# Performance work log

Measured on AMD Instinct MI355X. Metric: run time of the kernel, lower is better.

## Reference

```python
import jax, jax.numpy as jnp
import numpy as np

B, S, H = 4, 2048, 2048

def setup_inputs() -> dict:
    key = jax.random.key(0)
    k1, k2, k3 = jax.random.split(key, 3)
    xav_qkv = float(np.sqrt(6.0 / (H + 3 * H)))
    xav_out = float(np.sqrt(6.0 / (H + H)))
    return {
        "hidden_states": jax.random.normal(k1, (B, S, H), dtype=jnp.float32),
        "w_qkv": jax.random.uniform(k2, (3 * H, H), minval=-xav_qkv, maxval=xav_qkv, dtype=jnp.float32),
        "b_qkv": jnp.zeros((3 * H,), dtype=jnp.float32),
        "w_out": jax.random.uniform(k3, (H, H), minval=-xav_out, maxval=xav_out, dtype=jnp.float32),
        "b_out": jnp.zeros((H,), dtype=jnp.float32),
    }

def reference(hidden_states, w_qkv, b_qkv, w_out, b_out):
    Bc, Sc, Hc = hidden_states.shape
    scaling = jnp.sqrt(jnp.asarray(Hc, hidden_states.dtype))
    # qkv projection: torch Linear is x @ W^T + b
    qkv = jnp.einsum('bsh,oh->bso', hidden_states, w_qkv) + b_qkv  # [B,S,3H]
    q, k, v = jnp.split(qkv, 3, axis=-1)  # each [B,S,H]
    scores = jnp.einsum('bqh,bkh->bqk', q, k) / scaling  # [B,S,S]
    probs = jax.nn.softmax(scores, axis=-1)
    context = jnp.einsum('bqk,bkh->bqh', probs, v)  # [B,S,H]
    out = jnp.einsum('bsh,oh->bso', context, w_out) + b_out
    return out
```

## Files before the change

### kernel.cpp

```cpp
#include <hip/hip_runtime.h>
#include <cstdint>

typedef _Float16 f16;
typedef __attribute__((ext_vector_type(8))) _Float16 f16x8;
typedef __attribute__((ext_vector_type(4))) _Float16 f16x4;
typedef __attribute__((ext_vector_type(4))) float f32x4;

typedef __attribute__((address_space(1))) void gvoid_t;
typedef __attribute__((address_space(3))) void lvoid_t;

__device__ __forceinline__ void async_copy16(void* lds, const void* g) {
  __builtin_amdgcn_global_load_lds((gvoid_t*)(uintptr_t)g, (lvoid_t*)lds, 16, 0, 0);
}

#define BARRIER()   __builtin_amdgcn_s_barrier()
#define SCHEDBAR()  __builtin_amdgcn_sched_barrier(0)
#define LGKM0()     do { asm volatile("s_waitcnt lgkmcnt(0)" ::: "memory"); SCHEDBAR(); } while (0)
#define VMCNT(n)    do { SCHEDBAR(); asm volatile("s_waitcnt vmcnt(" #n ")"); SCHEDBAR(); } while (0)

#define MFMA16(a, b, c) __builtin_amdgcn_mfma_f32_16x16x32_f16((a), (b), (c), 0, 0, 0)

template<int OUT_F16>
__global__ __launch_bounds__(512, 2)
void gemm256(const f16* __restrict__ A, int lda, long sA,
             const f16* __restrict__ B, int ldb, long sB,
             void* __restrict__ Cv, int ldc, long sC,
             const float* __restrict__ bias, float scale, int K)
{
  __shared__ f16 AH0a[8192]; __shared__ f16 AH0b[8192];
  __shared__ f16 AH1a[8192]; __shared__ f16 AH1b[8192];
  __shared__ f16 BH0a[8192]; __shared__ f16 BH0b[8192];
  __shared__ f16 BH1a[8192]; __shared__ f16 BH1b[8192];

  const int tid = threadIdx.x, lane = tid & 63, wave = tid >> 6;
  const int wr = wave >> 2, wc = wave & 3;
  const int l15 = lane & 15, lk = lane >> 4;

  int lin = blockIdx.y * gridDim.x + blockIdx.x;
  const int nxy = gridDim.x * gridDim.y;
  if ((nxy & 7) == 0) lin = (lin & 7) * (nxy >> 3) + (lin >> 3);
  const int bx = lin % gridDim.x, by = lin / gridDim.x;

  const long brow = (long)by * 256, bcol = (long)bx * 256;
  const int z = blockIdx.z;
  const f16* Ab = A + (long)z * sA;
  const f16* Bb = B + (long)z * sB;

  const int r0  = tid >> 3;
  const int gc8 = (tid & 7) ^ (r0 & 7);
  const int sdst = wave * 512;

  const f16* gAa = Ab + (brow + r0) * (long)lda + gc8 * 8;
  const f16* gAb = gAa + 128L * lda;
  const f16* gBa = Bb + (bcol + r0) * (long)ldb + gc8 * 8;
  const f16* gBb = gBa + 128L * ldb;

#define STG(BUF, G, LD, KOFF) { \
    async_copy16(BUF + sdst,        (G) + (KOFF)); \
    async_copy16(BUF + 4096 + sdst, (G) + 64L * (LD) + (KOFF)); }

  const f16* myA0 = wr ? AH0b : AH0a;
  const f16* myA1 = wr ? AH1b : AH1a;
  const f16* myB0 = (wc & 2) ? BH0b : BH0a;
  const f16* myB1 = (wc & 2) ? BH1b : BH1a;

  const int x8   = l15 & 7;
  const int cb0  = (lk ^ x8) * 8;
  const int cb1  = ((4 | lk) ^ x8) * 8;
  const int lbA  = l15 * 64;
  const int lbB  = ((wc & 1) * 64 + l15) * 64;

#define RDA4(SRC, MP) { \
    af[0] = *(const f16x8*)&(SRC)[lbA + (2*(MP))   * 1024 + cb0]; \
    af[1] = *(const f16x8*)&(SRC)[lbA + (2*(MP))   * 1024 + cb1]; \
    af[2] = *(const f16x8*)&(SRC)[lbA + (2*(MP)+1) * 1024 + cb0]; \
    af[3] = *(const f16x8*)&(SRC)[lbA + (2*(MP)+1) * 1024 + cb1]; }

#define RDB8(SRC) { \
    bf[0][0] = *(const f16x8*)&(SRC)[lbB + 0 * 1024 + cb0]; \
    bf[1][0] = *(const f16x8*)&(SRC)[lbB + 0 * 1024 + cb1]; \
    bf[0][1] = *(const f16x8*)&(SRC)[lbB + 1 * 1024 + cb0]; \
    bf[1][1] = *(const f16x8*)&(SRC)[lbB + 1 * 1024 + cb1]; \
    bf[0][2] = *(const f16x8*)&(SRC)[lbB + 2 * 1024 + cb0]; \
    bf[1][2] = *(const f16x8*)&(SRC)[lbB + 2 * 1024 + cb1]; \
    bf[0][3] = *(const f16x8*)&(SRC)[lbB + 3 * 1024 + cb0]; \
    bf[1][3] = *(const f16x8*)&(SRC)[lbB + 3 * 1024 + cb1]; }

#define CLUSTER(MP) { \
    __builtin_amdgcn_s_setprio(1); \
    _Pragma("unroll") \
    for (int n = 0; n < 4; ++n) { \
      f32x4 t = MFMA16(af[0], bf[0][n], acc[2*(MP)][n]); \
      acc[2*(MP)][n] = MFMA16(af[1], bf[1][n], t); \
    } \
    _Pragma("unroll") \
    for (int n = 0; n < 4; ++n) { \
      f32x4 t = MFMA16(af[2], bf[0][n], acc[2*(MP)+1][n]); \
      acc[2*(MP)+1][n] = MFMA16(af[3], bf[1][n], t); \
    } \
    __builtin_amdgcn_s_setprio(0); }

  f32x4 acc[8][4] = {};
  f16x8 af[4], bf[2][4];
  const int NIT = K >> 7;

  STG(BH0a, gBa, ldb, 0);  STG(BH0b, gBb, ldb, 0);
  STG(AH0a, gAa, lda, 0);  STG(AH0b, gAb, lda, 0);
  STG(BH1a, gBa, ldb, 64); STG(BH1b, gBb, ldb, 64);
  VMCNT(4);
  BARRIER();

  for (int it = 0; it < NIT; ++it) {
    const long k1 = 128L * it + 64;
    const long k2 = k1 + 64, k3 = k1 + 128;
    const bool st = (it + 1 < NIT);

    RDA4(myA0, 0); RDB8(myB0);
    STG(AH1a, gAa, lda, k1);
    BARRIER(); LGKM0(); CLUSTER(0); BARRIER();

    RDA4(myA0, 1);
    STG(AH1b, gAb, lda, k1);
    BARRIER(); LGKM0(); CLUSTER(1); BARRIER();

    RDA4(myA0, 2);
    if (st) STG(BH0a, gBa, ldb, k2);
    BARRIER(); LGKM0(); CLUSTER(2); BARRIER();

    RDA4(myA0, 3);
    if (st) STG(BH0b, gBb, ldb, k2);
    BARRIER(); LGKM0(); CLUSTER(3);
    if (st) { VMCNT(4); } else { VMCNT(0); }
    BARRIER();

    RDA4(myA1, 0); RDB8(myB1);
    if (st) STG(AH0a, gAa, lda, k2);
    BARRIER(); LGKM0(); CLUSTER(0); BARRIER();

    RDA4(myA1, 1);
    if (st) STG(AH0b, gAb, lda, k2);
    BARRIER(); LGKM0(); CLUSTER(1); BARRIER();

    RDA4(myA1, 2);
    if (st) STG(BH1a, gBa, ldb, k3);
    BARRIER(); LGKM0(); CLUSTER(2); BARRIER();

    RDA4(myA1, 3);
    if (st) STG(BH1b, gBb, ldb, k3);
    BARRIER(); LGKM0(); CLUSTER(3);
    if (st) VMCNT(4);
    BARRIER();
  }

#pragma unroll
  for (int m = 0; m < 8; ++m) {
#pragma unroll
    for (int n = 0; n < 4; ++n) {
      const long col = bcol + wc * 64 + n * 16 + l15;
      const float bv = bias ? bias[col] : 0.0f;
#pragma unroll
      for (int j = 0; j < 4; ++j) {
        const long row = brow + wr * 128 + m * 16 + lk * 4 + j;
        const float v = acc[m][n][j] * scale + bv;
        if (OUT_F16)
          ((f16*)Cv)[(long)z * sC + row * ldc + col] = (f16)v;
        else
          ((float*)Cv)[(long)z * sC + row * ldc + col] = v;
      }
    }
  }
#undef STG
#undef RDA4
#undef RDB8
#undef CLUSTER
}

__global__ void cast_f32_f16(const float* __restrict__ in, f16* __restrict__ out, long n) {
  long i = ((long)blockIdx.x * blockDim.x + threadIdx.x) * 4;
  const long stride = (long)gridDim.x * blockDim.x * 4;
  for (; i < n; i += stride) {
    const float4 v = *reinterpret_cast<const float4*>(in + i);
    f16x4 h;
    h.x = (f16)v.x; h.y = (f16)v.y; h.z = (f16)v.z; h.w = (f16)v.w;
    *reinterpret_cast<f16x4*>(out + i) = h;
  }
}

__global__ __launch_bounds__(256)
void transpose_v(const f16* __restrict__ qkv, f16* __restrict__ vt) {
  __shared__ f16 t[32][33];
  const int b = blockIdx.z;
  const int s0 = blockIdx.y * 32, h0 = blockIdx.x * 32;
  const int tx = threadIdx.x, ty = threadIdx.y;
  const f16* src = qkv + (long)b * 2048 * 6144 + 4096;
  f16* dst = vt + (long)b * 2048 * 2048;
#pragma unroll
  for (int i = 0; i < 4; ++i)
    t[ty + i * 8][tx] = src[(long)(s0 + ty + i * 8) * 6144 + h0 + tx];
  __syncthreads();
#pragma unroll
  for (int i = 0; i < 4; ++i)
    dst[(long)(h0 + ty + i * 8) * 2048 + s0 + tx] = t[tx][ty + i * 8];
}

__global__ __launch_bounds__(256)
void softmax_rows(float* __restrict__ scores) {
  const long row = blockIdx.x;
  float* s = scores + row * 2048;
  const int tid = threadIdx.x;
  const int lane = tid & 63;
  const int wave = tid >> 6;

  const float4 a = *reinterpret_cast<const float4*>(s + tid * 8);
  const float4 b = *reinterpret_cast<const float4*>(s + tid * 8 + 4);
  float v[8] = {a.x, a.y, a.z, a.w, b.x, b.y, b.z, b.w};

  float mx = v[0];
#pragma unroll
  for (int j = 1; j < 8; ++j) mx = fmaxf(mx, v[j]);
#pragma unroll
  for (int off = 32; off >= 1; off >>= 1) mx = fmaxf(mx, __shfl_xor(mx, off));
  __shared__ float red[4];
  if (lane == 0) red[wave] = mx;
  __syncthreads();
  mx = fmaxf(fmaxf(red[0], red[1]), fmaxf(red[2], red[3]));

  float sum = 0.f;
#pragma unroll
  for (int j = 0; j < 8; ++j) { v[j] = __expf(v[j] - mx); sum += v[j]; }
#pragma unroll
  for (int off = 32; off >= 1; off >>= 1) sum += __shfl_xor(sum, off);
  __shared__ float red2[4];
  if (lane == 0) red2[wave] = sum;
  __syncthreads();
  const float inv = 1.0f / (red2[0] + red2[1] + red2[2] + red2[3]);

  f16* p = reinterpret_cast<f16*>(scores) + row * 4096 + tid * 8;
  f16x8 h;
#pragma unroll
  for (int j = 0; j < 8; ++j) h[j] = (f16)(v[j] * inv);
  *reinterpret_cast<f16x8*>(p) = h;
}

extern "C" void kernel_launch(void* const* d_in, const int* in_sizes, int n_in,
                              void* d_out, int out_size, void* d_ws, size_t ws_size,
                              hipStream_t stream) {
  const float* x     = (const float*)d_in[0];
  const float* w_qkv = (const float*)d_in[1];
  const float* b_qkv = (const float*)d_in[2];
  const float* w_out = (const float*)d_in[3];
  const float* b_out = (const float*)d_in[4];
  float* out = (float*)d_out;

  char* ws = (char*)d_ws;
  f16*   Xh    = (f16*)(ws + 0);
  f16*   Wqkvh = (f16*)(ws + 33554432L);
  f16*   Wouth = (f16*)(ws + 58720256L);
  f16*   QKV   = (f16*)(ws + 67108864L);
  float* SC    = (float*)(ws + 167772160L);
  f16*   VT    = (f16*)(ws + 234881024L);
  f16*   CTX   = Xh;

  const float inv_sqrt_h = 0.022097086912079608f;

  cast_f32_f16<<<2048, 256, 0, stream>>>(x,     Xh,    16777216L);
  cast_f32_f16<<<2048, 256, 0, stream>>>(w_qkv, Wqkvh, 12582912L);
  cast_f32_f16<<<1024, 256, 0, stream>>>(w_out, Wouth, 4194304L);

  gemm256<1><<<dim3(24, 32, 1), 512, 0, stream>>>(
      Xh, 2048, 0, Wqkvh, 2048, 0, QKV, 6144, 0, b_qkv, 1.0f, 2048);

  gemm256<0><<<dim3(8, 8, 4), 512, 0, stream>>>(
      QKV, 6144, 2048L * 6144, QKV + 2048, 6144, 2048L * 6144,
      SC, 2048, 2048L * 2048, nullptr, inv_sqrt_h, 2048);

  transpose_v<<<dim3(64, 64, 4), dim3(32, 8), 0, stream>>>(QKV, VT);

  softmax_rows<<<8192, 256, 0, stream>>>(SC);

  gemm256<1><<<dim3(8, 8, 4), 512, 0, stream>>>(
      (const f16*)SC, 4096, 2048L * 4096, VT, 2048, 2048L * 2048,
      CTX, 2048, 2048L * 2048, nullptr, 1.0f, 2048);

  gemm256<0><<<dim3(8, 32, 1), 512, 0, stream>>>(
      CTX, 2048, 0, Wouth, 2048, 0, out, 2048, 0, b_out, 1.0f, 2048);
}
```

Measured before the change: 478.7 us.

## Rotate GEMM stage loads and drop trailing barrier per compute cluster

Reorders the global-to-LDS staging sequence in the 256-tile GEMM main loop, shifting each half-tile load one cluster earlier and rotating BH1b into the loop head. It removes the second barrier after every MFMA cluster, halving barriers per iteration, and tightens the vmcnt waits to 2. The aim is less synchronisation stall and better overlap of async copies with MFMA work. The risk is an LDS race, since buffers may be overwritten before all waves finish reading them once the trailing barrier is gone.

```diff
diff --git a/kernel.cpp b/kernel.cpp
--- a/kernel.cpp
+++ b/kernel.cpp
@@ -106,50 +106,47 @@
 
   STG(BH0a, gBa, ldb, 0);  STG(BH0b, gBb, ldb, 0);
   STG(AH0a, gAa, lda, 0);  STG(AH0b, gAb, lda, 0);
-  STG(BH1a, gBa, ldb, 64); STG(BH1b, gBb, ldb, 64);
-  VMCNT(4);
+  STG(BH1a, gBa, ldb, 64);
+  VMCNT(2);
   BARRIER();
 
-  for (int it = 0; it < NIT; ++it) {
-    const long k1 = 128L * it + 64;
-    const long k2 = k1 + 64, k3 = k1 + 128;
-    const bool st = (it + 1 < NIT);
+  for (int J = 0; J < NIT; ++J) {
+    const long k1 = 128L * J + 64;
+    const long k2 = 128L * J + 128;
+    const long k3 = 128L * J + 192;
+    const bool st = (J + 1 < NIT);
 
     RDA4(myA0, 0); RDB8(myB0);
+    STG(BH1b, gBb, ldb, k1);
+    BARRIER(); LGKM0(); CLUSTER(0);
+
+    RDA4(myA0, 1);
     STG(AH1a, gAa, lda, k1);
-    BARRIER(); LGKM0(); CLUSTER(0); BARRIER();
-
-    RDA4(myA0, 1);
+    BARRIER(); LGKM0(); CLUSTER(1);
+
+    RDA4(myA0, 2);
     STG(AH1b, gAb, lda, k1);
-    BARRIER(); LGKM0(); CLUSTER(1); BARRIER();
-
-    RDA4(myA0, 2);
-    if (st) STG(BH0a, gBa, ldb, k2);
-    BARRIER(); LGKM0(); CLUSTER(2); BARRIER();
+    BARRIER(); LGKM0(); CLUSTER(2);
 
     RDA4(myA0, 3);
+    if (st) { STG(BH0a, gBa, ldb, k2); VMCNT(2); } else { VMCNT(0); }
+    BARRIER(); LGKM0(); CLUSTER(3);
+
+    RDA4(myA1, 0); RDB8(myB1);
     if (st) STG(BH0b, gBb, ldb, k2);
+    BARRIER(); LGKM0(); CLUSTER(0);
+
+    RDA4(myA1, 1);
+    if (st) STG(AH0a, gAa, lda, k2);
+    BARRIER(); LGKM0(); CLUSTER(1);
+
+    RDA4(myA1, 2);
+    if (st) STG(AH0b, gAb, lda, k2);
+    BARRIER(); LGKM0(); CLUSTER(2);
+
+    RDA4(myA1, 3);
+    if (st) { STG(BH1a, gBa, ldb, k3); VMCNT(2); }
     BARRIER(); LGKM0(); CLUSTER(3);
-    if (st) { VMCNT(4); } else { VMCNT(0); }
-    BARRIER();
-
-    RDA4(myA1, 0); RDB8(myB1);
-    if (st) STG(AH0a, gAa, lda, k2);
-    BARRIER(); LGKM0(); CLUSTER(0); BARRIER();
-
-    RDA4(myA1, 1);
-    if (st) STG(AH0b, gAb, lda, k2);
-    BARRIER(); LGKM0(); CLUSTER(1); BARRIER();
-
-    RDA4(myA1, 2);
-    if (st) STG(BH1a, gBa, ldb, k3);
-    BARRIER(); LGKM0(); CLUSTER(2); BARRIER();
-
-    RDA4(myA1, 3);
-    if (st) STG(BH1b, gBb, ldb, k3);
-    BARRIER(); LGKM0(); CLUSTER(3);
-    if (st) VMCNT(4);
-    BARRIER();
   }
 
 #pragma unroll
```

Result: faster. 461.1 us (-3.7%).
